# Kernel tuning notes

Hardware: AMD Instinct MI355X
Metric: run time of the kernel (lower is better)

Reference implementation:

```python
import jax, jax.numpy as jnp
import numpy as np

EMBED_DIM = 1024
NUM_HEADS = 16
HEAD_DIM = EMBED_DIM // NUM_HEADS
SCALE = float(np.sqrt(HEAD_DIM))
B, TQ, TK = 2, 2048, 2048


def setup_inputs() -> dict:
    key = jax.random.key(0)
    ks = jax.random.split(key, 16)
    s = 1.0 / np.sqrt(EMBED_DIM)
    inp = {
        "query": jax.random.normal(ks[0], (B, TQ, EMBED_DIM), jnp.float32),
        "key": jax.random.normal(ks[1], (B, TK, EMBED_DIM), jnp.float32),
        "value": jax.random.normal(ks[2], (B, TK, EMBED_DIM), jnp.float32),
        "key_padding_mask": jnp.zeros((B, TK), dtype=bool),
        "Wq": jax.random.uniform(ks[3], (EMBED_DIM, EMBED_DIM), jnp.float32, -s, s),
        "bq": jax.random.uniform(ks[4], (EMBED_DIM,), jnp.float32, -s, s),
        "Wk": jax.random.uniform(ks[5], (EMBED_DIM, EMBED_DIM), jnp.float32, -s, s),
        "bk": jax.random.uniform(ks[6], (EMBED_DIM,), jnp.float32, -s, s),
        "Wv": jax.random.uniform(ks[7], (EMBED_DIM, EMBED_DIM), jnp.float32, -s, s),
        "bv": jax.random.uniform(ks[8], (EMBED_DIM,), jnp.float32, -s, s),
        "Wo": jax.random.uniform(ks[9], (EMBED_DIM, EMBED_DIM), jnp.float32, -s, s),
        "bo": jax.random.uniform(ks[10], (EMBED_DIM,), jnp.float32, -s, s),
        "clr_bias_q": jax.random.normal(ks[11], (NUM_HEADS, 1, HEAD_DIM), jnp.float32) * 0.02,
        "clr_bias_k": jax.random.normal(ks[12], (NUM_HEADS, 1, HEAD_DIM), jnp.float32) * 0.02,
    }
    return inp


def reference(query, key, value, key_padding_mask, Wq, bq, Wk, bk, Wv, bv, Wo, bo,
              clr_bias_q, clr_bias_k):
    Bsz, Tq, _ = query.shape
    Tk = key.shape[1]

    def split_heads(x, W, b, T):
        # Linear (torch convention: x @ W.T + b) then [B, H, T, Dh]
        y = jnp.einsum('bte,fe->btf', x, W) + b
        return y.reshape(Bsz, T, NUM_HEADS, HEAD_DIM).transpose(0, 2, 1, 3)

    q = split_heads(query, Wq, bq, Tq)   # [B,H,Tq,Dh]
    k = split_heads(key, Wk, bk, Tk)     # [B,H,Tk,Dh]
    v = split_heads(value, Wv, bv, Tk)   # [B,H,Tk,Dh]

    # CLR centering + learned bias (Aitchison similarity)
    q_c = q - jnp.mean(q, axis=-1, keepdims=True) + clr_bias_q[None]
    k_c = k - jnp.mean(k, axis=-1, keepdims=True) + clr_bias_k[None]
    scores = jnp.einsum('bhqd,bhkd->bhqk', q_c, k_c) / SCALE  # [B,H,Tq,Tk]

    mask = key_padding_mask[:, None, None, :]  # [B,1,1,Tk], True = ignore
    scores = jnp.where(mask, -jnp.inf, scores)

    attn = jax.nn.softmax(scores, axis=-1)
    out = jnp.einsum('bhqk,bhkd->bhqd', attn, v)
    out = out.transpose(0, 2, 1, 3).reshape(Bsz, Tq, EMBED_DIM)
    return jnp.einsum('bte,fe->btf', out, Wo) + bo
```

## Files before the change

### kernel.cpp

```cpp
#include <hip/hip_runtime.h>
#include <stdint.h>

static constexpr int EMB   = 1024;
static constexpr int HEADS = 16;
static constexpr int HD    = 64;
static constexpr int BATCH = 2;
static constexpr int SEQ   = 2048;
static constexpr int BT    = BATCH * SEQ;
static constexpr float QSC = 0.18033688011112042f;

typedef short   short8  __attribute__((ext_vector_type(8)));
typedef float   float4v __attribute__((ext_vector_type(4)));

__device__ __forceinline__ ushort f2bf(float f) {
    union { float f; uint32_t i; } v; v.f = f;
    uint32_t x = v.i;
    return (ushort)((x + 0x7FFFu + ((x >> 16) & 1u)) >> 16);
}
__device__ __forceinline__ ushort f2bf_rn(float f) {
    union { float f; uint32_t i; } v; v.f = f;
    return (ushort)((v.i + 0x8000u) >> 16);
}
__device__ __forceinline__ uint32_t pack2bf(float lo, float hi) {
    union { float f; uint32_t u; } a, b; a.f = lo; b.f = hi;
    uint32_t ra = a.u + 0x7FFFu + ((a.u >> 16) & 1u);
    uint32_t rb = b.u + 0x7FFFu + ((b.u >> 16) & 1u);
    return (rb & 0xFFFF0000u) | (ra >> 16);
}
__device__ __forceinline__ float fast_exp2(float x) {
#if __has_builtin(__builtin_amdgcn_exp2f)
    return __builtin_amdgcn_exp2f(x);
#else
    return exp2f(x);
#endif
}

__device__ __forceinline__ void async_ld16(const void* g, void* l) {
    __builtin_amdgcn_global_load_lds(
        (const __attribute__((address_space(1))) void*)g,
        (__attribute__((address_space(3))) void*)l,
        16, 0, 0);
}

__global__ void cvt_all(const float* __restrict__ q, const float* __restrict__ k,
                        const float* __restrict__ v,
                        const float* __restrict__ wq, const float* __restrict__ wk,
                        const float* __restrict__ wv, const float* __restrict__ wo,
                        ushort* __restrict__ qb, ushort* __restrict__ kb,
                        ushort* __restrict__ vb,
                        ushort* __restrict__ wqb, ushort* __restrict__ wkb,
                        ushort* __restrict__ wvb, ushort* __restrict__ wob)
{
    int bid = blockIdx.x;
    const float* src; ushort* dst; size_t off;
    if (bid < 6144) {
        int seg = bid >> 11;
        src = seg == 0 ? q : (seg == 1 ? k : v);
        dst = seg == 0 ? qb : (seg == 1 ? kb : vb);
        off = (size_t)(bid & 2047) * 2048;
    } else {
        int t = bid - 6144, seg = t >> 9;
        src = seg == 0 ? wq : (seg == 1 ? wk : (seg == 2 ? wv : wo));
        dst = seg == 0 ? wqb : (seg == 1 ? wkb : (seg == 2 ? wvb : wob));
        off = (size_t)(t & 511) * 2048;
    }
    size_t base = off + (size_t)threadIdx.x * 8;
    float4 a0 = *(const float4*)(src + base);
    float4 a1 = *(const float4*)(src + base + 4);
    uint32_t o[4] = { pack2bf(a0.x, a0.y), pack2bf(a0.z, a0.w),
                      pack2bf(a1.x, a1.y), pack2bf(a1.z, a1.w) };
    *(uint4*)(dst + base) = *(uint4*)o;
}

__device__ __forceinline__ void gemm_core_128(
    const ushort* __restrict__ A, const ushort* __restrict__ W,
    int m0, int n0, int K,
    ushort* As, ushort* Ws,
    int wid, int lane, float4v acc[4][4])
{
    const int lrow8 = lane >> 3;
    const int gc    = (lane & 7) ^ lrow8;
    const ushort* Ab = A + (size_t)m0 * K + gc * 8;
    const ushort* Wb = W + (size_t)n0 * K + gc * 8;
    const int wm = (wid >> 1) * 64;
    const int wn = (wid & 1) * 64;

    for (int k0 = 0; k0 < K; k0 += 64) {
        __syncthreads();
#pragma unroll
        for (int it = 0; it < 4; ++it) {
            int rg = it * 4 + wid;
            int row = rg * 8 + lrow8;
            async_ld16(Ab + (size_t)row * K + k0, &As[rg * 512]);
            async_ld16(Wb + (size_t)row * K + k0, &Ws[rg * 512]);
        }
        __syncthreads();
#pragma unroll
        for (int ks = 0; ks < 2; ++ks) {
            const int c = ks * 4 + (lane >> 4);
            short8 af[4], wf[4];
#pragma unroll
            for (int i = 0; i < 4; i++) {
                int row = wm + i * 16 + (lane & 15);
                af[i] = *(const short8*)&As[row * 64 + ((c ^ (row & 7)) * 8)];
            }
#pragma unroll
            for (int j = 0; j < 4; j++) {
                int row = wn + j * 16 + (lane & 15);
                wf[j] = *(const short8*)&Ws[row * 64 + ((c ^ (row & 7)) * 8)];
            }
#pragma unroll
            for (int i = 0; i < 4; i++)
#pragma unroll
                for (int j = 0; j < 4; j++)
                    acc[i][j] = __builtin_amdgcn_mfma_f32_16x16x32_bf16(af[i], wf[j], acc[i][j], 0, 0, 0);
        }
    }
}

__global__ __launch_bounds__(256, 3)
void gemm_qkv(const ushort* __restrict__ qb, const ushort* __restrict__ kb,
              const ushort* __restrict__ vb,
              const ushort* __restrict__ wqb, const ushort* __restrict__ wkb,
              const ushort* __restrict__ wvb,
              const float* __restrict__ bq, const float* __restrict__ bk,
              const float* __restrict__ bv,
              const float* __restrict__ cbq, const float* __restrict__ cbk,
              ushort* __restrict__ qc, ushort* __restrict__ kc,
              ushort* __restrict__ vt)
{
    __shared__ __align__(16) ushort As[128 * 64];
    __shared__ __align__(16) ushort Ws[128 * 64];

    const int z = blockIdx.z;
    const ushort* A    = z == 0 ? qb  : (z == 1 ? kb  : vb);
    const ushort* W    = z == 0 ? wqb : (z == 1 ? wkb : wvb);
    const float*  bias = z == 0 ? bq  : (z == 1 ? bk  : bv);
    const float*  clrb = z == 0 ? cbq : cbk;
    const float   scale = z == 0 ? QSC : 1.0f;

    const int tid  = threadIdx.x;
    const int wid  = tid >> 6;
    const int lane = tid & 63;
    const int m0 = blockIdx.y * 128;
    const int n0 = blockIdx.x * 128;
    const int wm = (wid >> 1) * 64;
    const int wn = (wid & 1) * 64;

    float4v acc[4][4];
#pragma unroll
    for (int i = 0; i < 4; i++)
#pragma unroll
        for (int j = 0; j < 4; j++) acc[i][j] = (float4v)0.0f;

    gemm_core_128(A, W, m0, n0, EMB, As, Ws, wid, lane, acc);

    const int h = (n0 + wn) >> 6;
#pragma unroll
    for (int i = 0; i < 4; i++) {
        float ys[4][4];
#pragma unroll
        for (int j = 0; j < 4; j++) {
            float bj = bias[n0 + wn + j * 16 + (lane & 15)];
#pragma unroll
            for (int r = 0; r < 4; r++) ys[j][r] = acc[i][j][r] + bj;
        }
        const int rowb = m0 + wm + i * 16 + ((lane >> 4) << 2);

        if (z < 2) {
            float rs[4];
#pragma unroll
            for (int r = 0; r < 4; r++)
                rs[r] = ys[0][r] + ys[1][r] + ys[2][r] + ys[3][r];
#pragma unroll
            for (int r = 0; r < 4; r++)
#pragma unroll
                for (int off = 1; off < 16; off <<= 1)
                    rs[r] += __shfl_xor(rs[r], off, 64);
            ushort* Yb = z == 0 ? qc : kc;
#pragma unroll
            for (int j = 0; j < 4; j++) {
                int d = j * 16 + (lane & 15);
                float cb = clrb[h * HD + d];
#pragma unroll
                for (int r = 0; r < 4; r++) {
                    int row = rowb + r;
                    int b = row >> 11, t = row & (SEQ - 1);
                    Yb[((size_t)(b * HEADS + h) * SEQ + t) * HD + d] =
                        f2bf((ys[j][r] - rs[r] * (1.0f / 64.0f) + cb) * scale);
                }
            }
        } else {
#pragma unroll
            for (int j = 0; j < 4; j++) {
                int d = j * 16 + (lane & 15);
#pragma unroll
                for (int r = 0; r < 4; r++) {
                    int row = rowb + r;
                    int b = row >> 11, t = row & (SEQ - 1);
                    vt[((size_t)(b * HEADS + h) * HD + d) * SEQ + t] = f2bf(ys[j][r]);
                }
            }
        }
    }
}

__global__ __launch_bounds__(256, 3)
void gemm_out(const ushort* __restrict__ A, const ushort* __restrict__ W,
              const float* __restrict__ bias, float* __restrict__ Y)
{
    __shared__ __align__(16) ushort As[128 * 64];
    __shared__ __align__(16) ushort Ws[128 * 64];

    const int tid  = threadIdx.x;
    const int wid  = tid >> 6;
    const int lane = tid & 63;
    const int m0 = blockIdx.y * 128;
    const int n0 = blockIdx.x * 128;
    const int wm = (wid >> 1) * 64;
    const int wn = (wid & 1) * 64;

    float4v acc[4][4];
#pragma unroll
    for (int i = 0; i < 4; i++)
#pragma unroll
        for (int j = 0; j < 4; j++) acc[i][j] = (float4v)0.0f;

    gemm_core_128(A, W, m0, n0, EMB, As, Ws, wid, lane, acc);

#pragma unroll
    for (int i = 0; i < 4; i++) {
        const int rowb = m0 + wm + i * 16 + ((lane >> 4) << 2);
#pragma unroll
        for (int j = 0; j < 4; j++) {
            int col = n0 + wn + j * 16 + (lane & 15);
            float bj = bias[col];
#pragma unroll
            for (int r = 0; r < 4; r++)
                Y[(size_t)(rowb + r) * EMB + col] = acc[i][j][r] + bj;
        }
    }
}

__global__ __launch_bounds__(256, 3)
void attn_kernel(const ushort* __restrict__ qc,
                 const ushort* __restrict__ kc,
                 const ushort* __restrict__ vt,
                 const unsigned char* __restrict__ mask,
                 ushort* __restrict__ out)
{
    __shared__ __align__(16) ushort Ks[128 * 64];
    __shared__ __align__(16) ushort Vs[64 * 128];
    __shared__ __align__(16) ushort Ps[4][16 * 136];

    const int tid  = threadIdx.x;
    const int wid  = tid >> 6;
    const int lane = tid & 63;

    const int bid = blockIdx.x;
    const int qt = bid & 31;
    const int h  = (bid >> 5) & 15;
    const int b  = bid >> 9;

    const ushort* qbase = qc + ((size_t)(b * HEADS + h)) * SEQ * HD;
    const ushort* kbase = kc + ((size_t)(b * HEADS + h)) * SEQ * HD;
    const ushort* vbase = vt + ((size_t)(b * HEADS + h)) * HD * SEQ;

    const int qrow = qt * 64 + wid * 16 + (lane & 15);
    short8 qf[2];
#pragma unroll
    for (int ks = 0; ks < 2; ++ks)
        qf[ks] = *(const short8*)(qbase + (size_t)qrow * HD + ks * 32 + (lane >> 4) * 8);

    float l_r[4] = {0.f, 0.f, 0.f, 0.f};
    float4v o[4];
#pragma unroll
    for (int j = 0; j < 4; j++) o[j] = (float4v)0.f;

    const int lrow8 = lane >> 3;
    const int gcK   = (lane & 7) ^ lrow8;
    ushort* Pw = &Ps[wid][0];

    for (int kt = 0; kt < SEQ / 128; ++kt) {
        __syncthreads();
#pragma unroll
        for (int it = 0; it < 4; ++it) {
            int row = (it * 4 + wid) * 8 + lrow8;
            async_ld16(kbase + (size_t)(kt * 128 + row) * HD + gcK * 8,
                       &Ks[(it * 4 + wid) * 512]);
        }
#pragma unroll
        for (int it = 0; it < 4; ++it) {
            int row = (it * 4 + wid) * 4 + (lane >> 4);
            int gc  = (lane & 15) ^ (row & 15);
            async_ld16(vbase + (size_t)row * SEQ + kt * 128 + gc * 8,
                       &Vs[(it * 4 + wid) * 512]);
        }
        __syncthreads();

        float4v s[8];
#pragma unroll
        for (int j = 0; j < 8; j++) {
            s[j] = (float4v)0.f;
#pragma unroll
            for (int ks = 0; ks < 2; ks++) {
                int row = j * 16 + (lane & 15);
                int c   = ks * 4 + (lane >> 4);
                short8 kf = *(const short8*)&Ks[row * 64 + ((c ^ (row & 7)) * 8)];
                s[j] = __builtin_amdgcn_mfma_f32_16x16x32_bf16(qf[ks], kf, s[j], 0, 0, 0);
            }
        }

#pragma unroll
        for (int j = 0; j < 8; j++) {
            int key = kt * 128 + j * 16 + (lane & 15);
            float mz = mask[b * SEQ + key] ? -1e30f : 0.0f;
            int prow = ((lane >> 4) << 2) * 136 + j * 16 + (lane & 15);
#pragma unroll
            for (int r = 0; r < 4; r++) {
                float p = fast_exp2(s[j][r] + mz);
                l_r[r] += p;
                Pw[prow + r * 136] = f2bf_rn(p);
            }
        }
        asm volatile("s_waitcnt lgkmcnt(0)" ::: "memory");

        short8 pf[4];
#pragma unroll
        for (int ks = 0; ks < 4; ks++)
            pf[ks] = *(const short8*)&Pw[(lane & 15) * 136 + ks * 32 + (lane >> 4) * 8];

#pragma unroll
        for (int j = 0; j < 4; j++) {
            int d = j * 16 + (lane & 15);
#pragma unroll
            for (int ks = 0; ks < 4; ks++) {
                int c = ks * 4 + (lane >> 4);
                short8 vf = *(const short8*)&Vs[d * 128 + ((c ^ (d & 15)) * 8)];
                o[j] = __builtin_amdgcn_mfma_f32_16x16x32_bf16(pf[ks], vf, o[j], 0, 0, 0);
            }
        }
    }

#pragma unroll
    for (int r = 0; r < 4; r++)
#pragma unroll
        for (int off = 1; off < 16; off <<= 1)
            l_r[r] += __shfl_xor(l_r[r], off, 64);

    const int qrow_out = qt * 64 + wid * 16 + ((lane >> 4) << 2);
#pragma unroll
    for (int j = 0; j < 4; j++) {
        int d = j * 16 + (lane & 15);
#pragma unroll
        for (int r = 0; r < 4; r++) {
            float val = o[j][r] / l_r[r];
            out[((size_t)(b * SEQ + qrow_out + r)) * EMB + h * HD + d] = f2bf(val);
        }
    }
}

extern "C" void kernel_launch(void* const* d_in, const int* in_sizes, int n_in,
                              void* d_out, int out_size, void* d_ws, size_t ws_size,
                              hipStream_t stream)
{
    const float* query = (const float*)d_in[0];
    const float* key_  = (const float*)d_in[1];
    const float* value = (const float*)d_in[2];
    const unsigned char* mask = (const unsigned char*)d_in[3];
    const float* Wq  = (const float*)d_in[4];
    const float* bq  = (const float*)d_in[5];
    const float* Wk  = (const float*)d_in[6];
    const float* bk  = (const float*)d_in[7];
    const float* Wv  = (const float*)d_in[8];
    const float* bv  = (const float*)d_in[9];
    const float* Wo  = (const float*)d_in[10];
    const float* bo  = (const float*)d_in[11];
    const float* cbq = (const float*)d_in[12];
    const float* cbk = (const float*)d_in[13];

    ushort* ws = (ushort*)d_ws;
    const size_t n1 = (size_t)BT * EMB;
    const size_t nw = (size_t)EMB * EMB;
    ushort* qb  = ws;
    ushort* kb  = qb  + n1;
    ushort* vb  = kb  + n1;
    ushort* wqb = vb  + n1;
    ushort* wkb = wqb + nw;
    ushort* wvb = wkb + nw;
    ushort* wob = wvb + nw;
    ushort* qc  = wob + nw;
    ushort* kc  = qc  + n1;
    ushort* vt  = kc  + n1;
    ushort* ao  = qb;

    cvt_all<<<8192, 256, 0, stream>>>(query, key_, value, Wq, Wk, Wv, Wo,
                                      qb, kb, vb, wqb, wkb, wvb, wob);

    dim3 gq(EMB / 128, BT / 128, 3);
    gemm_qkv<<<gq, 256, 0, stream>>>(qb, kb, vb, wqb, wkb, wvb,
                                     bq, bk, bv, cbq, cbk, qc, kc, vt);

    attn_kernel<<<BATCH * HEADS * (SEQ / 64), 256, 0, stream>>>(qc, kc, vt, mask, ao);

    dim3 go(EMB / 128, BT / 128);
    gemm_out<<<go, 256, 0, stream>>>(ao, wob, bo, (float*)d_out);
}
```

Baseline: 249.8 us.

## Process two query sub-tiles per attention block to reuse K/V tiles

Each attention block now covers 128 query rows, with every wave computing two 16-row query sub-tiles against the same shared-memory K and V tile. This halves the K/V global-to-LDS traffic per query row and the number of blocks launched. In exchange, register pressure rises (double accumulators and Q fragments), launch bounds drop to 2 blocks per SM, and the grid shrinks to 512 blocks, which may underfill the GPU.

Result: slower. 261.8 us (+4.8%).

```diff
diff --git a/kernel.cpp b/kernel.cpp
--- a/kernel.cpp
+++ b/kernel.cpp
@@ -242,7 +242,7 @@
     }
 }
 
-__global__ __launch_bounds__(256, 3)
+__global__ __launch_bounds__(256, 2)
 void attn_kernel(const ushort* __restrict__ qc,
                  const ushort* __restrict__ kc,
                  const ushort* __restrict__ vt,
@@ -258,24 +258,29 @@
     const int lane = tid & 63;
 
     const int bid = blockIdx.x;
-    const int qt = bid & 31;
-    const int h  = (bid >> 5) & 15;
-    const int b  = bid >> 9;
+    const int qt = bid & 15;
+    const int h  = (bid >> 4) & 15;
+    const int b  = bid >> 8;
 
     const ushort* qbase = qc + ((size_t)(b * HEADS + h)) * SEQ * HD;
     const ushort* kbase = kc + ((size_t)(b * HEADS + h)) * SEQ * HD;
     const ushort* vbase = vt + ((size_t)(b * HEADS + h)) * HD * SEQ;
 
-    const int qrow = qt * 64 + wid * 16 + (lane & 15);
-    short8 qf[2];
-#pragma unroll
-    for (int ks = 0; ks < 2; ++ks)
-        qf[ks] = *(const short8*)(qbase + (size_t)qrow * HD + ks * 32 + (lane >> 4) * 8);
-
-    float l_r[4] = {0.f, 0.f, 0.f, 0.f};
-    float4v o[4];
-#pragma unroll
-    for (int j = 0; j < 4; j++) o[j] = (float4v)0.f;
+    short8 qf[2][2];
+#pragma unroll
+    for (int m = 0; m < 2; ++m) {
+        int qrow = qt * 128 + m * 64 + wid * 16 + (lane & 15);
+#pragma unroll
+        for (int ks = 0; ks < 2; ++ks)
+            qf[m][ks] = *(const short8*)(qbase + (size_t)qrow * HD + ks * 32 + (lane >> 4) * 8);
+    }
+
+    float l_r[2][4] = {{0.f,0.f,0.f,0.f},{0.f,0.f,0.f,0.f}};
+    float4v o[2][4];
+#pragma unroll
+    for (int m = 0; m < 2; ++m)
+#pragma unroll
+        for (int j = 0; j < 4; j++) o[m][j] = (float4v)0.f;
 
     const int lrow8 = lane >> 3;
     const int gcK   = (lane & 7) ^ lrow8;
@@ -298,64 +303,70 @@
         }
         __syncthreads();
 
-        float4v s[8];
-#pragma unroll
-        for (int j = 0; j < 8; j++) {
-            s[j] = (float4v)0.f;
-#pragma unroll
-            for (int ks = 0; ks < 2; ks++) {
-                int row = j * 16 + (lane & 15);
-                int c   = ks * 4 + (lane >> 4);
-                short8 kf = *(const short8*)&Ks[row * 64 + ((c ^ (row & 7)) * 8)];
-                s[j] = __builtin_amdgcn_mfma_f32_16x16x32_bf16(qf[ks], kf, s[j], 0, 0, 0);
-            }
-        }
-
-#pragma unroll
-        for (int j = 0; j < 8; j++) {
-            int key = kt * 128 + j * 16 + (lane & 15);
-            float mz = mask[b * SEQ + key] ? -1e30f : 0.0f;
-            int prow = ((lane >> 4) << 2) * 136 + j * 16 + (lane & 15);
-#pragma unroll
-            for (int r = 0; r < 4; r++) {
-                float p = fast_exp2(s[j][r] + mz);
-                l_r[r] += p;
-                Pw[prow + r * 136] = f2bf_rn(p);
-            }
-        }
-        asm volatile("s_waitcnt lgkmcnt(0)" ::: "memory");
-
-        short8 pf[4];
-#pragma unroll
-        for (int ks = 0; ks < 4; ks++)
-            pf[ks] = *(const short8*)&Pw[(lane & 15) * 136 + ks * 32 + (lane >> 4) * 8];
-
+#pragma unroll
+        for (int m = 0; m < 2; ++m) {
+            float4v s[8];
+#pragma unroll
+            for (int j = 0; j < 8; j++) {
+                s[j] = (float4v)0.f;
+#pragma unroll
+                for (int ks = 0; ks < 2; ks++) {
+                    int row = j * 16 + (lane & 15);
+                    int c   = ks * 4 + (lane >> 4);
+                    short8 kf = *(const short8*)&Ks[row * 64 + ((c ^ (row & 7)) * 8)];
+                    s[j] = __builtin_amdgcn_mfma_f32_16x16x32_bf16(qf[m][ks], kf, s[j], 0, 0, 0);
+                }
+            }
+
+#pragma unroll
+            for (int j = 0; j < 8; j++) {
+                int key = kt * 128 + j * 16 + (lane & 15);
+                float mz = mask[b * SEQ + key] ? -1e30f : 0.0f;
+                int prow = ((lane >> 4) << 2) * 136 + j * 16 + (lane & 15);
+#pragma unroll
+                for (int r = 0; r < 4; r++) {
+                    float p = fast_exp2(s[j][r] + mz);
+                    l_r[m][r] += p;
+                    Pw[prow + r * 136] = f2bf_rn(p);
+                }
+            }
+            asm volatile("s_waitcnt lgkmcnt(0)" ::: "memory");
+
+            short8 pf[4];
+#pragma unroll
+            for (int ks = 0; ks < 4; ks++)
+                pf[ks] = *(const short8*)&Pw[(lane & 15) * 136 + ks * 32 + (lane >> 4) * 8];
+
+#pragma unroll
+            for (int j = 0; j < 4; j++) {
+                int d = j * 16 + (lane & 15);
+#pragma unroll
+                for (int ks = 0; ks < 4; ks++) {
+                    int c = ks * 4 + (lane >> 4);
+                    short8 vf = *(const short8*)&Vs[d * 128 + ((c ^ (d & 15)) * 8)];
+                    o[m][j] = __builtin_amdgcn_mfma_f32_16x16x32_bf16(pf[ks], vf, o[m][j], 0, 0, 0);
+                }
+            }
+        }
+    }
+
+#pragma unroll
+    for (int m = 0; m < 2; ++m) {
+#pragma unroll
+        for (int r = 0; r < 4; r++)
+#pragma unroll
+            for (int off = 1; off < 16; off <<= 1)
+                l_r[m][r] += __shfl_xor(l_r[m][r], off, 64);
+
+        const int qrow_out = qt * 128 + m * 64 + wid * 16 + ((lane >> 4) << 2);
 #pragma unroll
         for (int j = 0; j < 4; j++) {
             int d = j * 16 + (lane & 15);
 #pragma unroll
-            for (int ks = 0; ks < 4; ks++) {
-                int c = ks * 4 + (lane >> 4);
-                short8 vf = *(const short8*)&Vs[d * 128 + ((c ^ (d & 15)) * 8)];
-                o[j] = __builtin_amdgcn_mfma_f32_16x16x32_bf16(pf[ks], vf, o[j], 0, 0, 0);
-            }
-        }
-    }
-
-#pragma unroll
-    for (int r = 0; r < 4; r++)
-#pragma unroll
-        for (int off = 1; off < 16; off <<= 1)
-            l_r[r] += __shfl_xor(l_r[r], off, 64);
-
-    const int qrow_out = qt * 64 + wid * 16 + ((lane >> 4) << 2);
-#pragma unroll
-    for (int j = 0; j < 4; j++) {
-        int d = j * 16 + (lane & 15);
-#pragma unroll
-        for (int r = 0; r < 4; r++) {
-            float val = o[j][r] / l_r[r];
-            out[((size_t)(b * SEQ + qrow_out + r)) * EMB + h * HD + d] = f2bf(val);
+            for (int r = 0; r < 4; r++) {
+                float val = o[m][j][r] / l_r[m][r];
+                out[((size_t)(b * SEQ + qrow_out + r)) * EMB + h * HD + d] = f2bf(val);
+            }
         }
     }
 }
@@ -401,7 +412,7 @@
     gemm_qkv<<<gq, 256, 0, stream>>>(qb, kb, vb, wqb, wkb, wvb,
                                      bq, bk, bv, cbq, cbk, qc, kc, vt);
 
-    attn_kernel<<<BATCH * HEADS * (SEQ / 64), 256, 0, stream>>>(qc, kc, vt, mask, ao);
+    attn_kernel<<<BATCH * HEADS * (SEQ / 128), 256, 0, stream>>>(qc, kc, vt, mask, ao);
 
     dim3 go(EMB / 128, BT / 128);
     gemm_out<<<go, 256, 0, stream>>>(ao, wob, bo, (float*)d_out);
```
